# Optimization experiments

Hardware: AMD Instinct MI355X
Metric: run time of the kernel (lower is better)

The kernel has to match this reference:

```python
import jax, jax.numpy as jnp
import numpy as np

D = 1024          # n_embd
E = 8             # n_experts
FF = 4 * D        # ffn hidden
CAP = 2048        # expert_capacity
W_IMP = 0.01
W_LOAD = 0.01
LAMBDA_Z = 0.001
W_PEN = 0.01
B, S = 4, 2048
T = B * S


def setup_inputs() -> dict:
    key = jax.random.key(0)
    ks = jax.random.split(key, 8)
    x = jax.random.normal(ks[0], (B, S, D), dtype=jnp.float32)
    gate_w = jax.random.normal(ks[1], (E, D), dtype=jnp.float32) * 0.02   # Linear(D,E) weight
    w1 = jax.random.normal(ks[2], (E, D, FF), dtype=jnp.float32) * 0.02   # c_fc weight per expert
    b1 = jnp.zeros((E, FF), dtype=jnp.float32)
    w2 = jax.random.normal(ks[3], (E, FF, D), dtype=jnp.float32) * 0.02   # c_proj weight per expert
    b2 = jnp.zeros((E, D), dtype=jnp.float32)
    rnd = jax.random.uniform(ks[4], (T,), dtype=jnp.float32)              # torch.rand_like(g2)
    return {"x": x, "gate_w": gate_w, "w1": w1, "b1": b1, "w2": w2, "b2": b2, "rnd": rnd}


def _dispatch_ffn_combine(xf, e_ids, pos, wts, mask, w1, b1, w2, b2):
    """Capacity-buffered dispatch -> grouped FFN -> weighted combine for one routing slot.
    xf: [T,D]; e_ids: [T] int; pos: [T] position within expert; wts: [T] combine weight
    (already zeroed where masked); mask: [T] bool within-capacity (and stochastic) mask."""
    pc = jnp.clip(pos, 0, CAP - 1)
    buf = jnp.zeros((E, CAP, xf.shape[-1]), xf.dtype)
    # masked tokens contribute zeros; valid positions are unique per expert so add == set
    buf = buf.at[e_ids, pc].add(xf * mask[:, None].astype(xf.dtype))
    h = jax.nn.gelu(jnp.einsum('ecd,edf->ecf', buf, w1) + b1[:, None, :], approximate=True)
    out = jnp.einsum('ecf,efd->ecd', h, w2) + b2[:, None, :]          # [E,C,D]
    return out[e_ids, pc] * wts[:, None]                               # [T,D]


def _forward(x, gate_w, w1, b1, w2, b2, rnd):
    xf = x.reshape(-1, x.shape[-1])                                    # [T,D]
    logits = xf @ gate_w.T                                             # [T,E] (bias=False)

    # auxiliary losses
    p166 = jax.nn.softmax(logits / 1.66, axis=-1)
    penalty_a = jnp.mean(p166 * (1.0 - p166))
    pm = p166.mean(axis=0)
    penalty_b = 1.0 / E - jnp.mean(pm * (1.0 - pm))
    penalty = W_PEN * (penalty_a + penalty_b)
    z_loss = LAMBDA_Z * jnp.mean(jax.nn.logsumexp(logits, axis=-1) ** 2)

    probs = jax.nn.softmax(logits.astype(jnp.float32), axis=-1).astype(x.dtype)
    weights, sel = jax.lax.top_k(probs, 2)
    g1, g2 = weights[:, 0], weights[:, 1]
    e1, e2 = sel[:, 0], sel[:, 1]
    denom = g1 + g2
    g1n, g2n = g1 / denom, g2 / denom

    oh1 = jax.nn.one_hot(e1, E, dtype=jnp.int32)
    pos1 = jnp.take_along_axis(jnp.cumsum(oh1, axis=0), e1[:, None], axis=1)[:, 0] - 1
    mask1 = pos1 < CAP
    w_slot1 = g1n * mask1.astype(x.dtype)

    oh2 = jax.nn.one_hot(e2, E, dtype=jnp.int32)
    pos2 = jnp.take_along_axis(jnp.cumsum(oh2, axis=0), e2[:, None], axis=1)[:, 0] - 1
    mask2 = (pos2 < CAP) & (rnd < 2.0 * g2n)
    w_slot2 = g2n * mask2.astype(x.dtype)

    # load-balance loss: f_i from top-1 one-hot, P_i from softmax probs
    f_i = oh1.astype(jnp.float32).mean(axis=0)
    P_i = probs.mean(axis=0)
    load_loss = W_LOAD * E * jnp.sum(f_i * P_i)

    # importance loss over combine matrix G (column sums)
    imp = jnp.zeros((E,), x.dtype).at[e1].add(w_slot1).at[e2].add(w_slot2)
    mean = imp.mean()
    var = jnp.var(imp)
    imp_loss = W_IMP * var / (mean ** 2)

    aux = penalty + z_loss + load_loss + imp_loss

    y = _dispatch_ffn_combine(xf, e1, pos1, w_slot1, mask1, w1, b1, w2, b2)
    y = y + _dispatch_ffn_combine(xf, e2, pos2, w_slot2, mask2, w1, b1, w2, b2)
    return y.reshape(x.shape), aux


def reference(x, gate_w, w1, b1, w2, b2, rnd):
    return _forward(x, gate_w, w1, b1, w2, b2, rnd)
```

## Files before the change

### kernel.cpp

```cpp
#include <hip/hip_runtime.h>
#include <math.h>
#include <stdint.h>

#define DD 1024
#define EE 8
#define FF 4096
#define CAPV 2048
#define TT 8192
#define LIST_STRIDE 4096

typedef __bf16 bf16x8 __attribute__((ext_vector_type(8)));
typedef __bf16 bf16x4 __attribute__((ext_vector_type(4)));
typedef float floatx4 __attribute__((ext_vector_type(4)));

typedef __attribute__((address_space(3))) unsigned int as3_uint;
typedef __attribute__((address_space(1))) const unsigned int as1_uint;

__device__ __forceinline__ void gl_lds16(const void* g, void* l) {
    __builtin_amdgcn_global_load_lds((as1_uint*)g, (as3_uint*)l, 16, 0, 0);
}

__device__ __forceinline__ unsigned short f2bf(float f) {
    union { float f; unsigned int u; } v; v.f = f;
    const unsigned int r = v.u + 0x7FFFu + ((v.u >> 16) & 1u);
    return (unsigned short)(r >> 16);
}

__global__ __launch_bounds__(256) void moe_gate_kernel(
    const float* __restrict__ x, const float* __restrict__ gw,
    int* __restrict__ e1o, int* __restrict__ e2o,
    float* __restrict__ g1o, float* __restrict__ g2o,
    float* __restrict__ sums, __bf16* __restrict__ xb)
{
    __shared__ float sgw[EE][DD];
    __shared__ float wp[4][26];
    for (int i = threadIdx.x; i < EE * DD; i += 256) sgw[i >> 10][i & 1023] = gw[i];
    __syncthreads();

    const int wave = threadIdx.x >> 6, lane = threadIdx.x & 63;
    const int gwave = blockIdx.x * 4 + wave;
    const int nwaves = gridDim.x * 4;

    float pa_acc = 0.f, z_acc = 0.f;
    float P_acc[EE] = {0}, p6_acc[EE] = {0};
    int n1_acc[EE] = {0};

    for (int t = gwave; t < TT; t += nwaves) {
        float acc[EE] = {0};
        const float* xr = x + (size_t)t * DD;
        __bf16* xbr = xb + (size_t)t * DD;
        #pragma unroll
        for (int i = 0; i < DD / 64; ++i) {
            const float xv = xr[lane + 64 * i];
            xbr[lane + 64 * i] = (__bf16)xv;
            #pragma unroll
            for (int e = 0; e < EE; ++e) acc[e] += xv * sgw[e][lane + 64 * i];
        }
        #pragma unroll
        for (int e = 0; e < EE; ++e) {
            float v = acc[e];
            #pragma unroll
            for (int off = 32; off > 0; off >>= 1) v += __shfl_xor(v, off, 64);
            acc[e] = v;
        }
        if (lane == 0) {
            float mx = acc[0];
            #pragma unroll
            for (int e = 1; e < EE; ++e) mx = fmaxf(mx, acc[e]);
            float pr[EE], p6[EE], se = 0.f, s6 = 0.f;
            #pragma unroll
            for (int e = 0; e < EE; ++e) {
                pr[e] = __expf(acc[e] - mx); se += pr[e];
                p6[e] = __expf((acc[e] - mx) * (1.0f / 1.66f)); s6 += p6[e];
            }
            const float lse = mx + __logf(se);
            z_acc += lse * lse;
            const float ise = 1.f / se, is6 = 1.f / s6;
            #pragma unroll
            for (int e = 0; e < EE; ++e) {
                pr[e] *= ise; p6[e] *= is6;
                P_acc[e] += pr[e]; p6_acc[e] += p6[e];
                pa_acc += p6[e] * (1.f - p6[e]);
            }
            int a = 0;
            #pragma unroll
            for (int e = 1; e < EE; ++e) if (pr[e] > pr[a]) a = e;
            int b = (a == 0) ? 1 : 0;
            #pragma unroll
            for (int e = 0; e < EE; ++e) if (e != a && pr[e] > pr[b]) b = e;
            n1_acc[a]++;
            const float ga = pr[a], gb = pr[b], idn = 1.f / (ga + gb);
            e1o[t] = a; e2o[t] = b;
            g1o[t] = ga * idn; g2o[t] = gb * idn;
        }
    }
    if (lane == 0) {
        wp[wave][0] = pa_acc; wp[wave][1] = z_acc;
        #pragma unroll
        for (int e = 0; e < EE; ++e) {
            wp[wave][2 + e] = P_acc[e]; wp[wave][10 + e] = p6_acc[e];
            wp[wave][18 + e] = (float)n1_acc[e];
        }
    }
    __syncthreads();
    if (threadIdx.x < 26) {
        const float s = wp[0][threadIdx.x] + wp[1][threadIdx.x] + wp[2][threadIdx.x] + wp[3][threadIdx.x];
        atomicAdd(&sums[threadIdx.x], s);
    }
}

__global__ __launch_bounds__(256) void moe_scan_kernel(
    const int* __restrict__ e1i, const int* __restrict__ e2i,
    const float* __restrict__ g1i, const float* __restrict__ g2i,
    const float* __restrict__ rnd, const float* __restrict__ sums,
    int* __restrict__ etok, int* __restrict__ p1o, int* __restrict__ p2o,
    int* __restrict__ cnt1, int* __restrict__ cnt2,
    float* __restrict__ imp1, float* __restrict__ imp2)
{
    const int bid = blockIdx.x, slot = bid >> 3, e = bid & 7;
    const int tid = threadIdx.x, wave = tid >> 6, lane = tid & 63;
    __shared__ int wtA[4], wtB[4];
    __shared__ float red[256];
    const int* ev = slot ? e2i : e1i;
    const float* gv = slot ? g2i : g1i;
    int* po = slot ? p2o : p1o;
    const int base = slot ? min((int)sums[18 + e], CAPV) : 0;

    int runTot = 0, runM = 0;
    float limp = 0.f;
    for (int c = 0; c < TT / 256; ++c) {
        const int t = c * 256 + tid;
        const int sel = (ev[t] == e) ? 1 : 0;
        const float w = gv[t];
        int ps = sel;
        #pragma unroll
        for (int off = 1; off < 64; off <<= 1) { int v = __shfl_up(ps, off, 64); if (lane >= off) ps += v; }
        if (lane == 63) wtA[wave] = ps;
        __syncthreads();
        int wpre = 0, ctot = 0;
        #pragma unroll
        for (int ww = 0; ww < 4; ++ww) { if (ww < wave) wpre += wtA[ww]; ctot += wtA[ww]; }
        const int pos = runTot + wpre + ps - 1;
        int m, idx;
        if (slot == 0) {
            m = sel && (pos < CAPV);
            idx = pos;
        } else {
            m = (sel && (pos < CAPV) && (rnd[t] < 2.f * w)) ? 1 : 0;
            int pm = m;
            #pragma unroll
            for (int off = 1; off < 64; off <<= 1) { int v = __shfl_up(pm, off, 64); if (lane >= off) pm += v; }
            if (lane == 63) wtB[wave] = pm;
            __syncthreads();
            int wpm = 0, mtot = 0;
            #pragma unroll
            for (int ww = 0; ww < 4; ++ww) { if (ww < wave) wpm += wtB[ww]; mtot += wtB[ww]; }
            idx = runM + wpm + pm - 1;
            runM += mtot;
        }
        if (sel) po[t] = m ? (e * LIST_STRIDE + base + idx) : -1;
        if (m) {
            etok[e * LIST_STRIDE + base + idx] = t;
            limp += w;
        }
        runTot += ctot;
        __syncthreads();
    }
    red[tid] = limp; __syncthreads();
    for (int s = 128; s > 0; s >>= 1) { if (tid < s) red[tid] += red[tid + s]; __syncthreads(); }
    if (tid == 0) {
        if (slot == 0) { cnt1[e] = min(runTot, CAPV); imp1[e] = red[0]; }
        else           { cnt2[e] = runM;              imp2[e] = red[0]; }
    }
}

__global__ void moe_aux_kernel(const float* __restrict__ sums,
                               const float* __restrict__ imp1, const float* __restrict__ imp2,
                               float* __restrict__ out_aux)
{
    if (threadIdx.x != 0 || blockIdx.x != 0) return;
    const float invT = 1.f / (float)TT;
    const float pa = sums[0] / ((float)TT * (float)EE);
    float pb = 0.f, load = 0.f, msum = 0.f;
    float im[EE];
    for (int e = 0; e < EE; ++e) {
        const float pm = sums[10 + e] * invT;
        pb += pm * (1.f - pm);
        load += (sums[18 + e] * invT) * (sums[2 + e] * invT);
        im[e] = imp1[e] + imp2[e];
        msum += im[e];
    }
    pb = 1.f / (float)EE - pb / (float)EE;
    const float penalty = 0.01f * (pa + pb);
    const float z_loss = 0.001f * sums[1] * invT;
    const float load_loss = 0.01f * (float)EE * load;
    const float mean = msum / (float)EE;
    float var = 0.f;
    for (int e = 0; e < EE; ++e) { const float d = im[e] - mean; var += d * d; }
    var /= (float)EE;
    const float imp_loss = 0.01f * var / (mean * mean);
    *out_aux = penalty + z_loss + load_loss + imp_loss;
}

__global__ __launch_bounds__(256) void transpose_bf16_kernel(
    const float* __restrict__ in, __bf16* __restrict__ out, int K, int N)
{
    __shared__ float tile[32][65];
    const int e = blockIdx.z;
    const float* ine = in + (size_t)e * K * N;
    __bf16* oute = out + (size_t)e * K * N;
    const int bk = blockIdx.x * 64, bn = blockIdx.y * 32;
    const int tid = threadIdx.x;
    #pragma unroll
    for (int p = 0; p < 8; ++p) {
        const int idx = p * 256 + tid;
        const int kl = idx >> 5, nl = idx & 31;
        tile[nl][kl] = ine[(size_t)(bk + kl) * N + bn + nl];
    }
    __syncthreads();
    #pragma unroll
    for (int p = 0; p < 4; ++p) {
        const int wdx = p * 256 + tid;
        const int nl = wdx >> 5, c = wdx & 31;
        const unsigned int pk = (unsigned int)f2bf(tile[nl][c * 2])
                              | ((unsigned int)f2bf(tile[nl][c * 2 + 1]) << 16);
        *(unsigned int*)&oute[(size_t)(bn + nl) * K + bk + c * 2] = pk;
    }
}

__global__ __launch_bounds__(256, 4) void moe_ffn1_mfma(
    const __bf16* __restrict__ xb, const __bf16* __restrict__ w1T,
    const float* __restrict__ b1, const int* __restrict__ etok,
    const int* __restrict__ cnt1, const int* __restrict__ cnt2,
    __bf16* __restrict__ H)
{
    const int f = blockIdx.x;
    const int xcd = f & 7, s = f >> 3;
    const int g = xcd * 32 + (s >> 5);
    const int e = g >> 5, n0 = (g & 31) * 128;
    const int m0 = (s & 31) * 128;
    const int ce = cnt1[e] + cnt2[e];
    if (m0 >= ce) return;
    const int tid = threadIdx.x, lane = tid & 63, w = tid >> 6;
    const int wm = w >> 1, wn = w & 1;

    __shared__ __bf16 As[2][4096];
    __shared__ __bf16 Bs[2][4096];

    const int csrc8 = (((tid & 3) ^ ((tid >> 3) & 3)) * 8);
    const int r0 = tid >> 2;
    const int gr0 = m0 + r0, gr1 = m0 + 64 + r0;
    const int tok0 = (gr0 < ce) ? etok[e * LIST_STRIDE + gr0] : 0;
    const int tok1 = (gr1 < ce) ? etok[e * LIST_STRIDE + gr1] : 0;
    const __bf16* aptr0 = xb + (size_t)tok0 * DD + csrc8;
    const __bf16* aptr1 = xb + (size_t)tok1 * DD + csrc8;
    const __bf16* bbase = w1T + (size_t)e * FF * DD;
    const __bf16* bptr0 = bbase + (size_t)(n0 + r0) * DD + csrc8;
    const __bf16* bptr1 = bbase + (size_t)(n0 + 64 + r0) * DD + csrc8;
    const int wofs = w * 512;

    floatx4 acc[4][4];
    #pragma unroll
    for (int i = 0; i < 4; ++i)
        #pragma unroll
        for (int j = 0; j < 4; ++j) acc[i][j] = floatx4{0.f, 0.f, 0.f, 0.f};

    const int quad = lane >> 4, l16 = lane & 15;
    const int swq = (quad ^ ((l16 >> 1) & 3)) * 8;

    gl_lds16(aptr0, &As[0][wofs]);
    gl_lds16(aptr1, &As[0][2048 + wofs]);
    gl_lds16(bptr0, &Bs[0][wofs]);
    gl_lds16(bptr1, &Bs[0][2048 + wofs]);

    int cur = 0;
    for (int k0 = 0; k0 < DD; k0 += 32) {
        __syncthreads();
        if (k0 + 32 < DD) {
            const int nb = cur ^ 1, kn = k0 + 32;
            gl_lds16(aptr0 + kn, &As[nb][wofs]);
            gl_lds16(aptr1 + kn, &As[nb][2048 + wofs]);
            gl_lds16(bptr0 + kn, &Bs[nb][wofs]);
            gl_lds16(bptr1 + kn, &Bs[nb][2048 + wofs]);
        }
        bf16x8 a[4], b[4];
        #pragma unroll
        for (int i = 0; i < 4; ++i)
            a[i] = *(const bf16x8*)&As[cur][(wm * 64 + i * 16 + l16) * 32 + swq];
        #pragma unroll
        for (int j = 0; j < 4; ++j)
            b[j] = *(const bf16x8*)&Bs[cur][(wn * 64 + j * 16 + l16) * 32 + swq];
        #pragma unroll
        for (int i = 0; i < 4; ++i)
            #pragma unroll
            for (int j = 0; j < 4; ++j)
                acc[i][j] = __builtin_amdgcn_mfma_f32_16x16x32_bf16(b[j], a[i], acc[i][j], 0, 0, 0);
        cur ^= 1;
    }

    const float* b1e = b1 + (size_t)e * FF;
    #pragma unroll
    for (int i = 0; i < 4; ++i) {
        const int mrow = m0 + wm * 64 + i * 16 + l16;
        __bf16* hrow = H + ((size_t)e * LIST_STRIDE + mrow) * FF;
        #pragma unroll
        for (int j = 0; j < 4; ++j) {
            const int col0 = n0 + wn * 64 + j * 16 + quad * 4;
            const float4 bb = *(const float4*)&b1e[col0];
            float vv[4] = {acc[i][j][0] + bb.x, acc[i][j][1] + bb.y,
                           acc[i][j][2] + bb.z, acc[i][j][3] + bb.w};
            bf16x4 pk;
            #pragma unroll
            for (int r = 0; r < 4; ++r) {
                const float v = vv[r];
                const float u = 0.7978845608028654f * (v + 0.044715f * v * v * v);
                const float th = 1.f - 2.f / (__expf(2.f * u) + 1.f);
                pk[r] = (__bf16)(0.5f * v * (1.f + th));
            }
            *(bf16x4*)&hrow[col0] = pk;
        }
    }
}

__global__ __launch_bounds__(256, 4) void moe_ffn2_mfma(
    const __bf16* __restrict__ H, const __bf16* __restrict__ w2T,
    const float* __restrict__ b2, const int* __restrict__ cnt1,
    const int* __restrict__ cnt2, __bf16* __restrict__ O)
{
    const int f = blockIdx.x;
    const int xcd = f & 7, s = f >> 3;
    const int g = xcd * 8 + (s >> 5);
    const int e = g >> 3, n0 = (g & 7) * 128;
    const int m0 = (s & 31) * 128;
    const int ce = cnt1[e] + cnt2[e];
    if (m0 >= ce) return;
    const int tid = threadIdx.x, lane = tid & 63, w = tid >> 6;
    const int wm = w >> 1, wn = w & 1;

    __shared__ __bf16 As[2][4096];
    __shared__ __bf16 Bs[2][4096];

    const int csrc8 = (((tid & 3) ^ ((tid >> 3) & 3)) * 8);
    const int r0 = tid >> 2;
    const __bf16* aptr0 = H + ((size_t)e * LIST_STRIDE + m0 + r0) * FF + csrc8;
    const __bf16* aptr1 = H + ((size_t)e * LIST_STRIDE + m0 + 64 + r0) * FF + csrc8;
    const __bf16* bbase = w2T + (size_t)e * DD * FF;
    const __bf16* bptr0 = bbase + (size_t)(n0 + r0) * FF + csrc8;
    const __bf16* bptr1 = bbase + (size_t)(n0 + 64 + r0) * FF + csrc8;
    const int wofs = w * 512;

    floatx4 acc[4][4];
    #pragma unroll
    for (int i = 0; i < 4; ++i)
        #pragma unroll
        for (int j = 0; j < 4; ++j) acc[i][j] = floatx4{0.f, 0.f, 0.f, 0.f};

    const int quad = lane >> 4, l16 = lane & 15;
    const int swq = (quad ^ ((l16 >> 1) & 3)) * 8;

    gl_lds16(aptr0, &As[0][wofs]);
    gl_lds16(aptr1, &As[0][2048 + wofs]);
    gl_lds16(bptr0, &Bs[0][wofs]);
    gl_lds16(bptr1, &Bs[0][2048 + wofs]);

    int cur = 0;
    for (int k0 = 0; k0 < FF; k0 += 32) {
        __syncthreads();
        if (k0 + 32 < FF) {
            const int nb = cur ^ 1, kn = k0 + 32;
            gl_lds16(aptr0 + kn, &As[nb][wofs]);
            gl_lds16(aptr1 + kn, &As[nb][2048 + wofs]);
            gl_lds16(bptr0 + kn, &Bs[nb][wofs]);
            gl_lds16(bptr1 + kn, &Bs[nb][2048 + wofs]);
        }
        bf16x8 a[4], b[4];
        #pragma unroll
        for (int i = 0; i < 4; ++i)
            a[i] = *(const bf16x8*)&As[cur][(wm * 64 + i * 16 + l16) * 32 + swq];
        #pragma unroll
        for (int j = 0; j < 4; ++j)
            b[j] = *(const bf16x8*)&Bs[cur][(wn * 64 + j * 16 + l16) * 32 + swq];
        #pragma unroll
        for (int i = 0; i < 4; ++i)
            #pragma unroll
            for (int j = 0; j < 4; ++j)
                acc[i][j] = __builtin_amdgcn_mfma_f32_16x16x32_bf16(b[j], a[i], acc[i][j], 0, 0, 0);
        cur ^= 1;
    }

    const float* b2e = b2 + (size_t)e * DD;
    #pragma unroll
    for (int i = 0; i < 4; ++i) {
        const int lrow = wm * 64 + i * 16 + l16;
        const int grow = m0 + lrow;
        if (grow < ce) {
            __bf16* orow = O + ((size_t)e * LIST_STRIDE + grow) * DD;
            #pragma unroll
            for (int j = 0; j < 4; ++j) {
                const int col0 = n0 + wn * 64 + j * 16 + quad * 4;
                const float4 bb = *(const float4*)&b2e[col0];
                bf16x4 pk;
                pk[0] = (__bf16)(acc[i][j][0] + bb.x);
                pk[1] = (__bf16)(acc[i][j][1] + bb.y);
                pk[2] = (__bf16)(acc[i][j][2] + bb.z);
                pk[3] = (__bf16)(acc[i][j][3] + bb.w);
                *(bf16x4*)&orow[col0] = pk;
            }
        }
    }
}

__global__ __launch_bounds__(256) void moe_combine_kernel(
    const __bf16* __restrict__ O, const float* __restrict__ g1v,
    const float* __restrict__ g2v, const int* __restrict__ p1v,
    const int* __restrict__ p2v, float* __restrict__ y)
{
    const int t = blockIdx.x;
    const int col = threadIdx.x * 4;
    const int p1 = p1v[t], p2 = p2v[t];
    float4 r = make_float4(0.f, 0.f, 0.f, 0.f);
    if (p1 >= 0) {
        const float g = g1v[t];
        const bf16x4 v = *(const bf16x4*)&O[(size_t)p1 * DD + col];
        r.x += g * (float)v[0]; r.y += g * (float)v[1];
        r.z += g * (float)v[2]; r.w += g * (float)v[3];
    }
    if (p2 >= 0) {
        const float g = g2v[t];
        const bf16x4 v = *(const bf16x4*)&O[(size_t)p2 * DD + col];
        r.x += g * (float)v[0]; r.y += g * (float)v[1];
        r.z += g * (float)v[2]; r.w += g * (float)v[3];
    }
    *(float4*)&y[(size_t)t * DD + col] = r;
}

extern "C" void kernel_launch(void* const* d_in, const int* in_sizes, int n_in,
                              void* d_out, int out_size, void* d_ws, size_t ws_size,
                              hipStream_t stream) {
    const float* x   = (const float*)d_in[0];
    const float* gw  = (const float*)d_in[1];
    const float* w1  = (const float*)d_in[2];
    const float* b1  = (const float*)d_in[3];
    const float* w2  = (const float*)d_in[4];
    const float* b2  = (const float*)d_in[5];
    const float* rnd = (const float*)d_in[6];
    float* out = (float*)d_out;

    char* p = (char*)d_ws;
    float* sums = (float*)p;
    float* imp1 = (float*)(p + 128);
    float* imp2 = (float*)(p + 160);
    int*   cnt1 = (int*)(p + 192);
    int*   cnt2 = (int*)(p + 224);
    p += 512;
    int*   e1v = (int*)p;   p += TT * 4;
    int*   e2v = (int*)p;   p += TT * 4;
    float* g1v = (float*)p; p += TT * 4;
    float* g2v = (float*)p; p += TT * 4;
    int*   p1v = (int*)p;   p += TT * 4;
    int*   p2v = (int*)p;   p += TT * 4;
    int*   etok = (int*)p;  p += EE * LIST_STRIDE * 4;
    uintptr_t q = (((uintptr_t)p) + 255) & ~(uintptr_t)255;
    __bf16* xb  = (__bf16*)q;  q += (size_t)TT * DD * 2;
    __bf16* w1T = (__bf16*)q;  q += (size_t)EE * FF * DD * 2;
    __bf16* w2T = (__bf16*)q;  q += (size_t)EE * DD * FF * 2;
    __bf16* H   = (__bf16*)q;  q += (size_t)EE * LIST_STRIDE * FF * 2;
    __bf16* O   = (__bf16*)q;

    hipMemsetAsync(sums, 0, 128, stream);

    moe_gate_kernel<<<256, 256, 0, stream>>>(x, gw, e1v, e2v, g1v, g2v, sums, xb);
    moe_scan_kernel<<<16, 256, 0, stream>>>(e1v, e2v, g1v, g2v, rnd, sums,
                                            etok, p1v, p2v, cnt1, cnt2, imp1, imp2);
    moe_aux_kernel<<<1, 64, 0, stream>>>(sums, imp1, imp2, out + (size_t)TT * DD);

    transpose_bf16_kernel<<<dim3(DD / 64, FF / 32, EE), 256, 0, stream>>>(w1, w1T, DD, FF);
    transpose_bf16_kernel<<<dim3(FF / 64, DD / 32, EE), 256, 0, stream>>>(w2, w2T, FF, DD);

    moe_ffn1_mfma<<<8192, 256, 0, stream>>>(xb, w1T, b1, etok, cnt1, cnt2, H);
    moe_ffn2_mfma<<<2048, 256, 0, stream>>>(H, w2T, b2, cnt1, cnt2, O);
    moe_combine_kernel<<<TT, 256, 0, stream>>>(O, g1v, g2v, p1v, p2v, out);
}
```

Baseline: 750.8 us.

## Enlarge expert GEMM tiles to 256x256 with 8 waves and BK=64 pipelining

Both expert FFN GEMMs now use 256x256 output tiles computed by 512-thread blocks of 8 waves, each wave owning a 128x64 sub-tile. The K step grows from 32 to 64 and uses a new XOR swizzle. Loads go through a double-buffered global-to-LDS pipeline with explicit vmcnt/lgkmcnt waits and raw barriers. The goal is more operand reuse per loaded byte and fewer barriers, at the cost of 128KB of LDS per block, fewer blocks in flight, more wasted work on partially filled expert tiles, and higher register pressure from the 32 accumulators.

```diff
diff --git a/kernel.cpp b/kernel.cpp
--- a/kernel.cpp
+++ b/kernel.cpp
@@ -228,7 +228,7 @@
     }
 }
 
-__global__ __launch_bounds__(256, 4) void moe_ffn1_mfma(
+__global__ __launch_bounds__(512, 2) void moe_ffn1_mfma(
     const __bf16* __restrict__ xb, const __bf16* __restrict__ w1T,
     const float* __restrict__ b1, const int* __restrict__ etok,
     const int* __restrict__ cnt1, const int* __restrict__ cnt2,
@@ -236,72 +236,102 @@
 {
     const int f = blockIdx.x;
     const int xcd = f & 7, s = f >> 3;
-    const int g = xcd * 32 + (s >> 5);
-    const int e = g >> 5, n0 = (g & 31) * 128;
-    const int m0 = (s & 31) * 128;
+    const int g = xcd * 16 + (s >> 4);
+    const int e = g >> 4, n0 = (g & 15) * 256;
+    const int m0 = (s & 15) * 256;
     const int ce = cnt1[e] + cnt2[e];
     if (m0 >= ce) return;
     const int tid = threadIdx.x, lane = tid & 63, w = tid >> 6;
-    const int wm = w >> 1, wn = w & 1;
-
-    __shared__ __bf16 As[2][4096];
-    __shared__ __bf16 Bs[2][4096];
-
-    const int csrc8 = (((tid & 3) ^ ((tid >> 3) & 3)) * 8);
-    const int r0 = tid >> 2;
-    const int gr0 = m0 + r0, gr1 = m0 + 64 + r0;
-    const int tok0 = (gr0 < ce) ? etok[e * LIST_STRIDE + gr0] : 0;
-    const int tok1 = (gr1 < ce) ? etok[e * LIST_STRIDE + gr1] : 0;
-    const __bf16* aptr0 = xb + (size_t)tok0 * DD + csrc8;
-    const __bf16* aptr1 = xb + (size_t)tok1 * DD + csrc8;
+    const int wm = w >> 2, wn = w & 3;
+    const int quad = lane >> 4, l16 = lane & 15;
+
+    __shared__ __bf16 As[2][16384];
+    __shared__ __bf16 Bs[2][16384];
+
+    const int srow = tid >> 3;
+    const int srcoff = ((tid & 7) ^ (srow & 7)) * 8;
+    const __bf16* ap[4];
+    const __bf16* bp[4];
     const __bf16* bbase = w1T + (size_t)e * FF * DD;
-    const __bf16* bptr0 = bbase + (size_t)(n0 + r0) * DD + csrc8;
-    const __bf16* bptr1 = bbase + (size_t)(n0 + 64 + r0) * DD + csrc8;
-    const int wofs = w * 512;
-
-    floatx4 acc[4][4];
-    #pragma unroll
-    for (int i = 0; i < 4; ++i)
+    #pragma unroll
+    for (int r = 0; r < 4; ++r) {
+        const int gr = m0 + r * 64 + srow;
+        const int tok = (gr < ce) ? etok[e * LIST_STRIDE + gr] : 0;
+        ap[r] = xb + (size_t)tok * DD + srcoff;
+        bp[r] = bbase + (size_t)(n0 + r * 64 + srow) * DD + srcoff;
+    }
+    const int ldst = w * 512;
+
+    floatx4 acc[8][4];
+    #pragma unroll
+    for (int i = 0; i < 8; ++i)
         #pragma unroll
         for (int j = 0; j < 4; ++j) acc[i][j] = floatx4{0.f, 0.f, 0.f, 0.f};
 
-    const int quad = lane >> 4, l16 = lane & 15;
-    const int swq = (quad ^ ((l16 >> 1) & 3)) * 8;
-
-    gl_lds16(aptr0, &As[0][wofs]);
-    gl_lds16(aptr1, &As[0][2048 + wofs]);
-    gl_lds16(bptr0, &Bs[0][wofs]);
-    gl_lds16(bptr1, &Bs[0][2048 + wofs]);
-
-    int cur = 0;
-    for (int k0 = 0; k0 < DD; k0 += 32) {
-        __syncthreads();
-        if (k0 + 32 < DD) {
-            const int nb = cur ^ 1, kn = k0 + 32;
-            gl_lds16(aptr0 + kn, &As[nb][wofs]);
-            gl_lds16(aptr1 + kn, &As[nb][2048 + wofs]);
-            gl_lds16(bptr0 + kn, &Bs[nb][wofs]);
-            gl_lds16(bptr1 + kn, &Bs[nb][2048 + wofs]);
-        }
-        bf16x8 a[4], b[4];
-        #pragma unroll
-        for (int i = 0; i < 4; ++i)
-            a[i] = *(const bf16x8*)&As[cur][(wm * 64 + i * 16 + l16) * 32 + swq];
-        #pragma unroll
-        for (int j = 0; j < 4; ++j)
-            b[j] = *(const bf16x8*)&Bs[cur][(wn * 64 + j * 16 + l16) * 32 + swq];
-        #pragma unroll
-        for (int i = 0; i < 4; ++i)
-            #pragma unroll
-            for (int j = 0; j < 4; ++j)
-                acc[i][j] = __builtin_amdgcn_mfma_f32_16x16x32_bf16(b[j], a[i], acc[i][j], 0, 0, 0);
-        cur ^= 1;
+    const int abase  = (wm * 128 + l16) * 64;
+    const int bbase2 = (wn * 64 + l16) * 64;
+    const int sw0 = (quad ^ (l16 & 7)) * 8;
+    const int sw1 = ((4 + quad) ^ (l16 & 7)) * 8;
+
+    auto stage = [&](int bufi, int koff) {
+        #pragma unroll
+        for (int r = 0; r < 4; ++r)
+            gl_lds16(ap[r] + koff, &As[bufi][r * 4096 + ldst]);
+        #pragma unroll
+        for (int r = 0; r < 4; ++r)
+            gl_lds16(bp[r] + koff, &Bs[bufi][r * 4096 + ldst]);
+    };
+    auto compute = [&](int bufi) {
+        bf16x8 bfr[4][2];
+        #pragma unroll
+        for (int j = 0; j < 4; ++j) {
+            bfr[j][0] = *(const bf16x8*)&Bs[bufi][bbase2 + j * 1024 + sw0];
+            bfr[j][1] = *(const bf16x8*)&Bs[bufi][bbase2 + j * 1024 + sw1];
+        }
+        #pragma unroll
+        for (int mh = 0; mh < 2; ++mh) {
+            bf16x8 av[4][2];
+            #pragma unroll
+            for (int i2 = 0; i2 < 4; ++i2) {
+                av[i2][0] = *(const bf16x8*)&As[bufi][abase + (mh * 4 + i2) * 1024 + sw0];
+                av[i2][1] = *(const bf16x8*)&As[bufi][abase + (mh * 4 + i2) * 1024 + sw1];
+            }
+            #pragma unroll
+            for (int i2 = 0; i2 < 4; ++i2)
+                #pragma unroll
+                for (int j = 0; j < 4; ++j) {
+                    floatx4 c = acc[mh * 4 + i2][j];
+                    c = __builtin_amdgcn_mfma_f32_16x16x32_bf16(bfr[j][0], av[i2][0], c, 0, 0, 0);
+                    c = __builtin_amdgcn_mfma_f32_16x16x32_bf16(bfr[j][1], av[i2][1], c, 0, 0, 0);
+                    acc[mh * 4 + i2][j] = c;
+                }
+        }
+    };
+
+    stage(0, 0);
+    stage(1, 64);
+    asm volatile("s_waitcnt vmcnt(8)" ::: "memory");
+    __builtin_amdgcn_s_barrier();
+
+    #pragma unroll 2
+    for (int t = 0; t < 16; ++t) {
+        const int cur = t & 1;
+        compute(cur);
+        asm volatile("s_waitcnt lgkmcnt(0)" ::: "memory");
+        __builtin_amdgcn_s_barrier();
+        if (t < 14) {
+            stage(cur, (t + 2) * 64);
+            asm volatile("s_waitcnt vmcnt(8)" ::: "memory");
+        } else {
+            asm volatile("s_waitcnt vmcnt(0)" ::: "memory");
+        }
+        __builtin_amdgcn_s_barrier();
     }
 
     const float* b1e = b1 + (size_t)e * FF;
     #pragma unroll
-    for (int i = 0; i < 4; ++i) {
-        const int mrow = m0 + wm * 64 + i * 16 + l16;
+    for (int i = 0; i < 8; ++i) {
+        const int mrow = m0 + wm * 128 + i * 16 + l16;
         __bf16* hrow = H + ((size_t)e * LIST_STRIDE + mrow) * FF;
         #pragma unroll
         for (int j = 0; j < 4; ++j) {
@@ -322,77 +352,107 @@
     }
 }
 
-__global__ __launch_bounds__(256, 4) void moe_ffn2_mfma(
+__global__ __launch_bounds__(512, 2) void moe_ffn2_mfma(
     const __bf16* __restrict__ H, const __bf16* __restrict__ w2T,
     const float* __restrict__ b2, const int* __restrict__ cnt1,
     const int* __restrict__ cnt2, __bf16* __restrict__ O)
 {
     const int f = blockIdx.x;
     const int xcd = f & 7, s = f >> 3;
-    const int g = xcd * 8 + (s >> 5);
-    const int e = g >> 3, n0 = (g & 7) * 128;
-    const int m0 = (s & 31) * 128;
+    const int g = xcd * 4 + (s >> 4);
+    const int e = g >> 2, n0 = (g & 3) * 256;
+    const int m0 = (s & 15) * 256;
     const int ce = cnt1[e] + cnt2[e];
     if (m0 >= ce) return;
     const int tid = threadIdx.x, lane = tid & 63, w = tid >> 6;
-    const int wm = w >> 1, wn = w & 1;
-
-    __shared__ __bf16 As[2][4096];
-    __shared__ __bf16 Bs[2][4096];
-
-    const int csrc8 = (((tid & 3) ^ ((tid >> 3) & 3)) * 8);
-    const int r0 = tid >> 2;
-    const __bf16* aptr0 = H + ((size_t)e * LIST_STRIDE + m0 + r0) * FF + csrc8;
-    const __bf16* aptr1 = H + ((size_t)e * LIST_STRIDE + m0 + 64 + r0) * FF + csrc8;
+    const int wm = w >> 2, wn = w & 3;
+    const int quad = lane >> 4, l16 = lane & 15;
+
+    __shared__ __bf16 As[2][16384];
+    __shared__ __bf16 Bs[2][16384];
+
+    const int srow = tid >> 3;
+    const int srcoff = ((tid & 7) ^ (srow & 7)) * 8;
+    const __bf16* ap[4];
+    const __bf16* bp[4];
     const __bf16* bbase = w2T + (size_t)e * DD * FF;
-    const __bf16* bptr0 = bbase + (size_t)(n0 + r0) * FF + csrc8;
-    const __bf16* bptr1 = bbase + (size_t)(n0 + 64 + r0) * FF + csrc8;
-    const int wofs = w * 512;
-
-    floatx4 acc[4][4];
-    #pragma unroll
-    for (int i = 0; i < 4; ++i)
+    #pragma unroll
+    for (int r = 0; r < 4; ++r) {
+        ap[r] = H + ((size_t)e * LIST_STRIDE + m0 + r * 64 + srow) * FF + srcoff;
+        bp[r] = bbase + (size_t)(n0 + r * 64 + srow) * FF + srcoff;
+    }
+    const int ldst = w * 512;
+
+    floatx4 acc[8][4];
+    #pragma unroll
+    for (int i = 0; i < 8; ++i)
         #pragma unroll
         for (int j = 0; j < 4; ++j) acc[i][j] = floatx4{0.f, 0.f, 0.f, 0.f};
 
-    const int quad = lane >> 4, l16 = lane & 15;
-    const int swq = (quad ^ ((l16 >> 1) & 3)) * 8;
-
-    gl_lds16(aptr0, &As[0][wofs]);
-    gl_lds16(aptr1, &As[0][2048 + wofs]);
-    gl_lds16(bptr0, &Bs[0][wofs]);
-    gl_lds16(bptr1, &Bs[0][2048 + wofs]);
-
-    int cur = 0;
-    for (int k0 = 0; k0 < FF; k0 += 32) {
-        __syncthreads();
-        if (k0 + 32 < FF) {
-            const int nb = cur ^ 1, kn = k0 + 32;
-            gl_lds16(aptr0 + kn, &As[nb][wofs]);
-            gl_lds16(aptr1 + kn, &As[nb][2048 + wofs]);
-            gl_lds16(bptr0 + kn, &Bs[nb][wofs]);
-            gl_lds16(bptr1 + kn, &Bs[nb][2048 + wofs]);
-        }
-        bf16x8 a[4], b[4];
-        #pragma unroll
-        for (int i = 0; i < 4; ++i)
-            a[i] = *(const bf16x8*)&As[cur][(wm * 64 + i * 16 + l16) * 32 + swq];
-        #pragma unroll
-        for (int j = 0; j < 4; ++j)
-            b[j] = *(const bf16x8*)&Bs[cur][(wn * 64 + j * 16 + l16) * 32 + swq];
-        #pragma unroll
-        for (int i = 0; i < 4; ++i)
-            #pragma unroll
-            for (int j = 0; j < 4; ++j)
-                acc[i][j] = __builtin_amdgcn_mfma_f32_16x16x32_bf16(b[j], a[i], acc[i][j], 0, 0, 0);
-        cur ^= 1;
+    const int abase  = (wm * 128 + l16) * 64;
+    const int bbase2 = (wn * 64 + l16) * 64;
+    const int sw0 = (quad ^ (l16 & 7)) * 8;
+    const int sw1 = ((4 + quad) ^ (l16 & 7)) * 8;
+
+    auto stage = [&](int bufi, int koff) {
+        #pragma unroll
+        for (int r = 0; r < 4; ++r)
+            gl_lds16(ap[r] + koff, &As[bufi][r * 4096 + ldst]);
+        #pragma unroll
+        for (int r = 0; r < 4; ++r)
+            gl_lds16(bp[r] + koff, &Bs[bufi][r * 4096 + ldst]);
+    };
+    auto compute = [&](int bufi) {
+        bf16x8 bfr[4][2];
+        #pragma unroll
+        for (int j = 0; j < 4; ++j) {
+            bfr[j][0] = *(const bf16x8*)&Bs[bufi][bbase2 + j * 1024 + sw0];
+            bfr[j][1] = *(const bf16x8*)&Bs[bufi][bbase2 + j * 1024 + sw1];
+        }
+        #pragma unroll
+        for (int mh = 0; mh < 2; ++mh) {
+            bf16x8 av[4][2];
+            #pragma unroll
+            for (int i2 = 0; i2 < 4; ++i2) {
+                av[i2][0] = *(const bf16x8*)&As[bufi][abase + (mh * 4 + i2) * 1024 + sw0];
+                av[i2][1] = *(const bf16x8*)&As[bufi][abase + (mh * 4 + i2) * 1024 + sw1];
+            }
+            #pragma unroll
+            for (int i2 = 0; i2 < 4; ++i2)
+                #pragma unroll
+                for (int j = 0; j < 4; ++j) {
+                    floatx4 c = acc[mh * 4 + i2][j];
+                    c = __builtin_amdgcn_mfma_f32_16x16x32_bf16(bfr[j][0], av[i2][0], c, 0, 0, 0);
+                    c = __builtin_amdgcn_mfma_f32_16x16x32_bf16(bfr[j][1], av[i2][1], c, 0, 0, 0);
+                    acc[mh * 4 + i2][j] = c;
+                }
+        }
+    };
+
+    stage(0, 0);
+    stage(1, 64);
+    asm volatile("s_waitcnt vmcnt(8)" ::: "memory");
+    __builtin_amdgcn_s_barrier();
+
+    #pragma unroll 2
+    for (int t = 0; t < 64; ++t) {
+        const int cur = t & 1;
+        compute(cur);
+        asm volatile("s_waitcnt lgkmcnt(0)" ::: "memory");
+        __builtin_amdgcn_s_barrier();
+        if (t < 62) {
+            stage(cur, (t + 2) * 64);
+            asm volatile("s_waitcnt vmcnt(8)" ::: "memory");
+        } else {
+            asm volatile("s_waitcnt vmcnt(0)" ::: "memory");
+        }
+        __builtin_amdgcn_s_barrier();
     }
 
     const float* b2e = b2 + (size_t)e * DD;
     #pragma unroll
-    for (int i = 0; i < 4; ++i) {
-        const int lrow = wm * 64 + i * 16 + l16;
-        const int grow = m0 + lrow;
+    for (int i = 0; i < 8; ++i) {
+        const int grow = m0 + wm * 128 + i * 16 + l16;
         if (grow < ce) {
             __bf16* orow = O + ((size_t)e * LIST_STRIDE + grow) * DD;
             #pragma unroll
@@ -477,7 +537,7 @@
     transpose_bf16_kernel<<<dim3(DD / 64, FF / 32, EE), 256, 0, stream>>>(w1, w1T, DD, FF);
     transpose_bf16_kernel<<<dim3(FF / 64, DD / 32, EE), 256, 0, stream>>>(w2, w2T, FF, DD);
 
-    moe_ffn1_mfma<<<8192, 256, 0, stream>>>(xb, w1T, b1, etok, cnt1, cnt2, H);
-    moe_ffn2_mfma<<<2048, 256, 0, stream>>>(H, w2T, b2, cnt1, cnt2, O);
+    moe_ffn1_mfma<<<2048, 512, 0, stream>>>(xb, w1T, b1, etok, cnt1, cnt2, H);
+    moe_ffn2_mfma<<<512, 512, 0, stream>>>(H, w2T, b2, cnt1, cnt2, O);
     moe_combine_kernel<<<TT, 256, 0, stream>>>(O, g1v, g2v, p1v, p2v, out);
 }
```

After: 711.6 us. -5.2%, faster.
